# Kernel optimization log

Hardware: AMD Instinct MI355X
Metric: run time of the kernel (lower is better)

## Reference

```python
import jax, jax.numpy as jnp
import numpy as np

D_MODEL = 1024
N_HEADS = 16


def setup_inputs() -> dict:
    key = jax.random.key(0)
    ks = jax.random.split(key, 7)
    scale = 1.0 / np.sqrt(D_MODEL)
    seq = jax.random.normal(ks[0], (4, 1024, D_MODEL), dtype=jnp.float32)
    Wq = jax.random.normal(ks[1], (D_MODEL, D_MODEL), dtype=jnp.float32) * scale
    bq = jax.random.normal(ks[2], (D_MODEL,), dtype=jnp.float32) * 0.02
    Wk = jax.random.normal(ks[3], (D_MODEL, D_MODEL), dtype=jnp.float32) * scale
    bk = jax.random.normal(ks[4], (D_MODEL,), dtype=jnp.float32) * 0.02
    Wv = jax.random.normal(ks[5], (D_MODEL, D_MODEL), dtype=jnp.float32) * scale
    bv = jax.random.normal(ks[6], (D_MODEL,), dtype=jnp.float32) * 0.02
    return {"seq": seq, "Wq": Wq, "bq": bq, "Wk": Wk, "bk": bk, "Wv": Wv, "bv": bv}


def reference(seq, Wq, bq, Wk, bk, Wv, bv):
    B, S, D = seq.shape
    H = N_HEADS
    dv = D // H
    # nn.Linear: x @ W.T + b; W stored [out, in]
    q = (seq @ Wq.T + bq).reshape(B, S, H, dv).transpose(0, 2, 1, 3)  # [B,H,S,dv]
    k = (seq @ Wk.T + bk).reshape(B, S, H, dv).transpose(0, 2, 1, 3)
    v = (seq @ Wv.T + bv).reshape(B, S, H, dv).transpose(0, 2, 1, 3)
    scores = jnp.einsum('bhqd,bhkd->bhqk', q, k) / jnp.sqrt(jnp.asarray(dv, seq.dtype))
    p = jax.nn.softmax(scores, axis=-1)
    out = jnp.einsum('bhqk,bhkd->bhqd', p, v)  # [B,H,S,dv]
    return out.transpose(0, 2, 1, 3).reshape(B, S, D)
```

## Files before the change

### kernel.cpp

```cpp
#include <hip/hip_runtime.h>
#include <hip/hip_fp16.h>

typedef _Float16 f16x8 __attribute__((ext_vector_type(8)));
typedef _Float16 f16x4 __attribute__((ext_vector_type(4)));
typedef float f32x4 __attribute__((ext_vector_type(4)));

#define D_MODEL 1024
#define SEQ 1024
#define BATCH 4
#define NH 16
#define DV 64
#define M_TOTAL (BATCH * SEQ)
#define QBLK 128

__device__ __forceinline__ void gload16(const _Float16* g, _Float16* lds) {
    __builtin_amdgcn_global_load_lds((const __attribute__((address_space(1))) void*)g,
                                     (__attribute__((address_space(3))) void*)lds,
                                     16, 0, 0);
}

__global__ void cvt_f32_f16(const float* __restrict__ s, _Float16* __restrict__ d, int n) {
    int i = (blockIdx.x * blockDim.x + threadIdx.x) * 8;
    if (i >= n) return;
    float4 a = *(const float4*)(s + i);
    float4 b = *(const float4*)(s + i + 4);
    f16x8 h;
    h[0] = (_Float16)a.x; h[1] = (_Float16)a.y; h[2] = (_Float16)a.z; h[3] = (_Float16)a.w;
    h[4] = (_Float16)b.x; h[5] = (_Float16)b.y; h[6] = (_Float16)b.z; h[7] = (_Float16)b.w;
    *(f16x8*)(d + i) = h;
}

__global__ void cvt3_f32_f16(const float* __restrict__ s0, const float* __restrict__ s1,
                             const float* __restrict__ s2, _Float16* __restrict__ d0,
                             _Float16* __restrict__ d1, _Float16* __restrict__ d2, int n) {
    const float* s = (blockIdx.y == 0) ? s0 : (blockIdx.y == 1 ? s1 : s2);
    _Float16*    d = (blockIdx.y == 0) ? d0 : (blockIdx.y == 1 ? d1 : d2);
    int i = (blockIdx.x * blockDim.x + threadIdx.x) * 8;
    if (i >= n) return;
    float4 a = *(const float4*)(s + i);
    float4 b = *(const float4*)(s + i + 4);
    f16x8 h;
    h[0] = (_Float16)a.x; h[1] = (_Float16)a.y; h[2] = (_Float16)a.z; h[3] = (_Float16)a.w;
    h[4] = (_Float16)b.x; h[5] = (_Float16)b.y; h[6] = (_Float16)b.z; h[7] = (_Float16)b.w;
    *(f16x8*)(d + i) = h;
}

__global__ __launch_bounds__(512, 2) void qkv_gemm(
    const _Float16* __restrict__ X,
    const _Float16* __restrict__ W0, const _Float16* __restrict__ W1, const _Float16* __restrict__ W2,
    const float* __restrict__ b0, const float* __restrict__ b1, const float* __restrict__ b2,
    _Float16* __restrict__ Qo, _Float16* __restrict__ Ko, _Float16* __restrict__ Vto)
{
    __shared__ _Float16 SM[4 * 256 * 64];
#define ABASE(buf) (SM + (buf) * 16384)
#define BBASE(buf) (SM + 32768 + (buf) * 16384)

    const int tid = threadIdx.x;
    const int l = tid & 63;
    const int w = tid >> 6;
    const int wr = w >> 2, wc = w & 3;

    const int bid = blockIdx.x;
    const int nid = (bid & 7) * 24 + (bid >> 3);
    const int mt = nid & 15, ntg = nid >> 4;
    const int mat = ntg >> 2, nt = ntg & 3;
    const _Float16* Wm  = (mat == 0) ? W0 : (mat == 1 ? W1 : W2);
    const float*    bia = (mat == 0) ? b0 : (mat == 1 ? b1 : b2);
    const int m0 = mt * 256, n0 = nt * 256;

    const int str = tid >> 3;
    const int sc8 = ((tid & 7) ^ (str & 7)) * 8;
    const _Float16* xsrc = X  + (size_t)(m0 + str) * D_MODEL + sc8;
    const _Float16* wsrc = Wm + (size_t)(n0 + str) * D_MODEL + sc8;
    const int ldst = str * 64 + (tid & 7) * 8;

#define SA(buf, kt, h) do { \
    gload16(xsrc + (size_t)((h) * 128) * D_MODEL + (kt) * 64, ABASE(buf) + (h) * 8192 + ldst); \
    gload16(xsrc + (size_t)((h) * 128 + 64) * D_MODEL + (kt) * 64, ABASE(buf) + (h) * 8192 + 4096 + ldst); } while (0)
#define SB(buf, kt, h) do { \
    gload16(wsrc + (size_t)((h) * 128) * D_MODEL + (kt) * 64, BBASE(buf) + (h) * 8192 + ldst); \
    gload16(wsrc + (size_t)((h) * 128 + 64) * D_MODEL + (kt) * 64, BBASE(buf) + (h) * 8192 + 4096 + ldst); } while (0)

    const int fr = l & 15, g = l >> 4, fr7 = l & 7;
    const int wrow = wr * 128, bcol = wc * 64;

    f32x4 acc[8][4] = {};
    f16x8 b[4][2];

    SB(0, 0, 0); SB(0, 0, 1);
    SA(0, 0, 0); SA(0, 0, 1);
    SB(1, 1, 0); SB(1, 1, 1);
    asm volatile("s_waitcnt vmcnt(4)" ::: "memory");
    __builtin_amdgcn_s_barrier();

#define PHASES(BUF, TSA_BUF, TSA, TSB_BUF, TSB)                                              \
    _Pragma("unroll")                                                                        \
    for (int p = 0; p < 4; ++p) {                                                            \
        if (p == 0) {                                                                        \
            _Pragma("unroll")                                                                \
            for (int nj = 0; nj < 4; ++nj) {                                                 \
                const int rb = (bcol + nj * 16 + fr) * 64;                                   \
                b[nj][0] = *(const f16x8*)&BBASE(BUF)[rb + ((g ^ fr7) << 3)];                \
                b[nj][1] = *(const f16x8*)&BBASE(BUF)[rb + (((4 + g) ^ fr7) << 3)];          \
            }                                                                                \
        }                                                                                    \
        f16x8 aq[2][2];                                                                      \
        _Pragma("unroll")                                                                    \
        for (int q = 0; q < 2; ++q) {                                                        \
            const int ra = (wrow + (2 * p + q) * 16 + fr) * 64;                              \
            aq[q][0] = *(const f16x8*)&ABASE(BUF)[ra + ((g ^ fr7) << 3)];                    \
            aq[q][1] = *(const f16x8*)&ABASE(BUF)[ra + (((4 + g) ^ fr7) << 3)];              \
        }                                                                                    \
        if (p == 0) SA(TSA_BUF, TSA, 0);                                                     \
        else if (p == 1) SA(TSA_BUF, TSA, 1);                                                \
        else if (p == 2) SB(TSB_BUF, TSB, 0);                                                \
        else SB(TSB_BUF, TSB, 1);                                                            \
        __builtin_amdgcn_s_barrier();                                                        \
        __builtin_amdgcn_s_setprio(1);                                                       \
        _Pragma("unroll")                                                                    \
        for (int ks = 0; ks < 2; ++ks)                                                       \
            _Pragma("unroll")                                                                \
            for (int q = 0; q < 2; ++q)                                                      \
                _Pragma("unroll")                                                            \
                for (int nj = 0; nj < 4; ++nj)                                               \
                    acc[2 * p + q][nj] = __builtin_amdgcn_mfma_f32_16x16x32_f16(             \
                        aq[q][ks], b[nj][ks], acc[2 * p + q][nj], 0, 0, 0);                  \
        __builtin_amdgcn_s_setprio(0);                                                       \
        if (p == 3) asm volatile("s_waitcnt vmcnt(4)" ::: "memory");                         \
        __builtin_amdgcn_s_barrier();                                                        \
    }

    for (int it = 0; it < 8; ++it) {
        const int tA = 2 * it + 1;
        const int tN = (2 * it + 2 < 16) ? 2 * it + 2 : 15;
        const int tM = (2 * it + 3 < 16) ? 2 * it + 3 : 15;
        PHASES(0, 1, tA, 0, tN)
        PHASES(1, 0, tN, 1, tM)
    }
#undef PHASES
#undef SA
#undef SB

    if (mat != 2) {
        const float scale = (mat == 0) ? 0.125f * 1.44269504088896340736f : 1.0f;
#pragma unroll
        for (int nj = 0; nj < 4; ++nj) {
            const int o = n0 + bcol + nj * 16 + fr;
            const float bb = bia[o];
            const int h = o >> 6, dd = o & 63;
#pragma unroll
            for (int mi = 0; mi < 8; ++mi) {
#pragma unroll
                for (int r = 0; r < 4; ++r) {
                    const int m = m0 + wrow + mi * 16 + g * 4 + r;
                    const int bi = m >> 10, s = m & 1023;
                    const float v = (acc[mi][nj][r] + bb) * scale;
                    const _Float16 hv = (_Float16)v;
                    const int bh = bi * NH + h;
                    if (mat == 0) Qo[((size_t)bh * SEQ + s) * DV + dd] = hv;
                    else          Ko[((size_t)bh * SEQ + s) * DV + dd] = hv;
                }
            }
        }
    } else {
        asm volatile("s_waitcnt vmcnt(0)" ::: "memory");
        __syncthreads();
#pragma unroll
        for (int nj = 0; nj < 4; ++nj) {
            const int n = bcol + nj * 16 + fr;
            const float bb = bia[n0 + n];
#pragma unroll
            for (int mi = 0; mi < 8; ++mi) {
#pragma unroll
                for (int r = 0; r < 4; ++r) {
                    const int m = wrow + mi * 16 + g * 4 + r;
                    SM[n * 256 + ((((m >> 3) + n) & 31) << 3) + (m & 7)] =
                        (_Float16)(acc[mi][nj][r] + bb);
                }
            }
        }
        __syncthreads();
        const int bi = m0 >> 10, s0 = m0 & 1023;
#pragma unroll
        for (int itp = 0; itp < 16; ++itp) {
            const int task = itp * 512 + tid;
            const int dd = task >> 5, sc = task & 31;
            f16x8 vv = *(const f16x8*)&SM[dd * 256 + (((sc + dd) & 31) << 3)];
            const int og = n0 + dd;
            const int h = og >> 6, d = og & 63;
            const int bh = bi * NH + h;
            *(f16x8*)(Vto + ((size_t)bh * DV + d) * SEQ + s0 + sc * 8) = vv;
        }
    }
#undef ABASE
#undef BBASE
}

__global__ __launch_bounds__(256) void attn(
    const _Float16* __restrict__ Q, const _Float16* __restrict__ K,
    const _Float16* __restrict__ Vt, float* __restrict__ out)
{
    __shared__ _Float16 Kb[2][64 * 64];
    __shared__ _Float16 Vb[2][64 * 64];
    __shared__ _Float16 P[4][2][16][80];

    const int w = threadIdx.x >> 6, l = threadIdx.x & 63;
    const int qc = l & 15, g = l >> 4;

    const int fid = blockIdx.y * 8 + blockIdx.x;
    const int nid = (fid & 7) * 64 + (fid >> 3);
    const int bh = nid >> 3, qt = nid & 7;
    const int b = bh >> 4, h = bh & 15;
    const int q0 = qt * QBLK + w * 32;

    const int r8 = l >> 3;
    const int cs = ((l & 7) ^ r8) * 8;
    const _Float16* Kg = K  + (size_t)bh * SEQ * DV;
    const _Float16* Vg = Vt + (size_t)bh * DV * SEQ;

    f16x8 qf[2][2];
#pragma unroll
    for (int qg = 0; qg < 2; ++qg) {
        const _Float16* qp = Q + ((size_t)bh * SEQ + q0 + qg * 16 + qc) * DV + g * 8;
        qf[qg][0] = *(const f16x8*)(qp);
        qf[qg][1] = *(const f16x8*)(qp + 32);
    }

    float m_run[2] = {-1e30f, -1e30f}, l_run[2] = {0.f, 0.f};
    f32x4 oacc[2][4] = {};

#define STAGE(buf, kb)                                                          \
    {                                                                           \
        _Float16* kd = &Kb[buf][(w * 8) * 64];                                  \
        _Float16* vd = &Vb[buf][(w * 8) * 64];                                  \
        const int row = w * 8 + r8;                                             \
        gload16(Kg + (size_t)((kb) + row) * DV + cs, kd);                       \
        gload16(Kg + (size_t)((kb) + row + 32) * DV + cs, kd + 32 * 64);        \
        gload16(Vg + (size_t)row * SEQ + (kb) + cs, vd);                        \
        gload16(Vg + (size_t)(row + 32) * SEQ + (kb) + cs, vd + 32 * 64);       \
    }

    STAGE(0, 0);
    __syncthreads();

    for (int kt = 0; kt < 16; ++kt) {
        const int ct = kt & 1;
        if (kt < 15) STAGE(ct ^ 1, (kt + 1) * 64);
        const _Float16* Ktile = Kb[ct];
        const _Float16* Vtile = Vb[ct];

#pragma unroll
        for (int qg = 0; qg < 2; ++qg) {
            f32x4 sT[4];
            const f32x4 zf = {0.f, 0.f, 0.f, 0.f};
            __builtin_amdgcn_s_setprio(1);
#pragma unroll
            for (int kf = 0; kf < 4; ++kf) {
                const int row = kf * 16 + qc;
                f16x8 ka0 = *(const f16x8*)&Ktile[row * 64 + (((g)     ^ (qc & 7)) << 3)];
                f16x8 ka1 = *(const f16x8*)&Ktile[row * 64 + (((4 + g) ^ (qc & 7)) << 3)];
                f32x4 t = __builtin_amdgcn_mfma_f32_16x16x32_f16(ka0, qf[qg][0], zf, 0, 0, 0);
                sT[kf] = __builtin_amdgcn_mfma_f32_16x16x32_f16(ka1, qf[qg][1], t, 0, 0, 0);
            }
            __builtin_amdgcn_s_setprio(0);
            f32x4 mx = sT[0];
#pragma unroll
            for (int kf = 1; kf < 4; ++kf)
#pragma unroll
                for (int r = 0; r < 4; ++r) mx[r] = fmaxf(mx[r], sT[kf][r]);
            float pmax = fmaxf(fmaxf(mx[0], mx[1]), fmaxf(mx[2], mx[3]));
            pmax = fmaxf(pmax, __shfl_xor(pmax, 16));
            pmax = fmaxf(pmax, __shfl_xor(pmax, 32));
            if (!__all(pmax - m_run[qg] <= 8.0f)) {
                const float mn = fmaxf(m_run[qg], pmax);
                const float al = exp2f(m_run[qg] - mn);
                l_run[qg] *= al;
#pragma unroll
                for (int df = 0; df < 4; ++df) oacc[qg][df] *= al;
                m_run[qg] = mn;
            }
            float rsum = 0.f;
#pragma unroll
            for (int kf = 0; kf < 4; ++kf) {
                f16x4 ph;
#pragma unroll
                for (int r = 0; r < 4; ++r) {
                    const float p = exp2f(sT[kf][r] - m_run[qg]);
                    rsum += p;
                    ph[r] = (_Float16)p;
                }
                *(f16x4*)&P[w][qg][qc][kf * 16 + g * 4] = ph;
            }
            rsum += __shfl_xor(rsum, 16);
            rsum += __shfl_xor(rsum, 32);
            l_run[qg] += rsum;

            __builtin_amdgcn_s_setprio(1);
#pragma unroll
            for (int ks = 0; ks < 2; ++ks) {
                f16x8 pb = *(const f16x8*)&P[w][qg][qc][ks * 32 + g * 8];
#pragma unroll
                for (int df = 0; df < 4; ++df) {
                    const int row = df * 16 + qc;
                    f16x8 va = *(const f16x8*)&Vtile[row * 64 + (((ks * 4 + g) ^ (qc & 7)) << 3)];
                    oacc[qg][df] = __builtin_amdgcn_mfma_f32_16x16x32_f16(va, pb, oacc[qg][df], 0, 0, 0);
                }
            }
            __builtin_amdgcn_s_setprio(0);
        }
        __syncthreads();
    }
#undef STAGE

#pragma unroll
    for (int qg = 0; qg < 2; ++qg) {
        const float inv = 1.0f / l_run[qg];
        float* ob = out + ((size_t)b * SEQ + q0 + qg * 16 + qc) * D_MODEL + h * DV;
#pragma unroll
        for (int df = 0; df < 4; ++df) {
            float4 v4;
            v4.x = oacc[qg][df][0] * inv; v4.y = oacc[qg][df][1] * inv;
            v4.z = oacc[qg][df][2] * inv; v4.w = oacc[qg][df][3] * inv;
            *(float4*)(ob + df * 16 + g * 4) = v4;
        }
    }
}

extern "C" void kernel_launch(void* const* d_in, const int* in_sizes, int n_in,
                              void* d_out, int out_size, void* d_ws, size_t ws_size,
                              hipStream_t stream) {
    const float* seq = (const float*)d_in[0];
    const float* Wq  = (const float*)d_in[1];
    const float* bq  = (const float*)d_in[2];
    const float* Wk  = (const float*)d_in[3];
    const float* bk  = (const float*)d_in[4];
    const float* Wv  = (const float*)d_in[5];
    const float* bv  = (const float*)d_in[6];
    float* out = (float*)d_out;

    _Float16* seqh = (_Float16*)d_ws;
    _Float16* wqh  = seqh + (size_t)M_TOTAL * D_MODEL;
    _Float16* wkh  = wqh + (size_t)D_MODEL * D_MODEL;
    _Float16* wvh  = wkh + (size_t)D_MODEL * D_MODEL;
    _Float16* Qh   = wvh + (size_t)D_MODEL * D_MODEL;
    _Float16* Kh   = Qh + (size_t)M_TOTAL * D_MODEL;
    _Float16* Vth  = Kh + (size_t)M_TOTAL * D_MODEL;

    const int n_seq = M_TOTAL * D_MODEL;
    const int n_w   = D_MODEL * D_MODEL;
    cvt_f32_f16<<<n_seq / (256 * 8), 256, 0, stream>>>(seq, seqh, n_seq);
    cvt3_f32_f16<<<dim3(n_w / (256 * 8), 3), 256, 0, stream>>>(Wq, Wk, Wv, wqh, wkh, wvh, n_w);

    qkv_gemm<<<192, 512, 0, stream>>>(
        seqh, wqh, wkh, wvh, bq, bk, bv, Qh, Kh, Vth);

    attn<<<dim3(SEQ / QBLK, BATCH * NH), 256, 0, stream>>>(Qh, Kh, Vth, out);
}
```

Baseline: 91.81 us.

## Split attention KV range across two wave groups and pass P via lane shuffles

The attention kernel doubles to 512 threads. Two groups of four waves each process half of the key/value sequence for the same query block, and their partial softmax states are merged at the end through shared memory (split-K flash attention). The P matrix is converted with packed cvt_pkrtz and redistributed into MFMA operand layout through cross-lane shuffles instead of an LDS round trip. Both query groups' QK and PV MFMAs are interleaved for more independent instructions. The intent is to raise occupancy and latency hiding. The cost is more LDS, a final merge step, and extra shuffle work.

```diff
diff --git a/kernel.cpp b/kernel.cpp
--- a/kernel.cpp
+++ b/kernel.cpp
@@ -17,6 +17,13 @@
     __builtin_amdgcn_global_load_lds((const __attribute__((address_space(1))) void*)g,
                                      (__attribute__((address_space(3))) void*)lds,
                                      16, 0, 0);
+}
+
+__device__ __forceinline__ unsigned pk16(float a, float b) {
+    auto h = __builtin_amdgcn_cvt_pkrtz(a, b);
+    unsigned r;
+    __builtin_memcpy(&r, &h, 4);
+    return r;
 }
 
 __global__ void cvt_f32_f16(const float* __restrict__ s, _Float16* __restrict__ d, int n) {
@@ -196,27 +203,33 @@
 #undef BBASE
 }
 
-__global__ __launch_bounds__(256) void attn(
+__global__ __launch_bounds__(512, 4) void attn(
     const _Float16* __restrict__ Q, const _Float16* __restrict__ K,
     const _Float16* __restrict__ Vt, float* __restrict__ out)
 {
-    __shared__ _Float16 Kb[2][64 * 64];
-    __shared__ _Float16 Vb[2][64 * 64];
-    __shared__ _Float16 P[4][2][16][80];
-
-    const int w = threadIdx.x >> 6, l = threadIdx.x & 63;
+    __shared__ _Float16 Kb[2][2][64 * 64];
+    __shared__ _Float16 Vb[2][2][64 * 64];
+    __shared__ float MLb[4][2][16][2];
+
+    const int tid = threadIdx.x;
+    const int w = tid >> 6, l = tid & 63;
+    const int grp = w >> 2, wl = w & 3;
     const int qc = l & 15, g = l >> 4;
+    const int g0 = g & 1, g1 = g >> 1;
 
     const int fid = blockIdx.y * 8 + blockIdx.x;
     const int nid = (fid & 7) * 64 + (fid >> 3);
     const int bh = nid >> 3, qt = nid & 7;
     const int b = bh >> 4, h = bh & 15;
-    const int q0 = qt * QBLK + w * 32;
-
-    const int r8 = l >> 3;
-    const int cs = ((l & 7) ^ r8) * 8;
+    const int q0 = qt * QBLK + wl * 32;
+
+    const int gt = tid & 255;
+    const int srow = gt >> 3;
+    const int scs = ((gt & 7) ^ (srow & 7)) * 8;
+    const int ldst = srow * 64 + (gt & 7) * 8;
     const _Float16* Kg = K  + (size_t)bh * SEQ * DV;
     const _Float16* Vg = Vt + (size_t)bh * DV * SEQ;
+    const int kbase = grp * 512;
 
     f16x8 qf[2][2];
 #pragma unroll
@@ -229,45 +242,47 @@
     float m_run[2] = {-1e30f, -1e30f}, l_run[2] = {0.f, 0.f};
     f32x4 oacc[2][4] = {};
 
-#define STAGE(buf, kb)                                                          \
-    {                                                                           \
-        _Float16* kd = &Kb[buf][(w * 8) * 64];                                  \
-        _Float16* vd = &Vb[buf][(w * 8) * 64];                                  \
-        const int row = w * 8 + r8;                                             \
-        gload16(Kg + (size_t)((kb) + row) * DV + cs, kd);                       \
-        gload16(Kg + (size_t)((kb) + row + 32) * DV + cs, kd + 32 * 64);        \
-        gload16(Vg + (size_t)row * SEQ + (kb) + cs, vd);                        \
-        gload16(Vg + (size_t)(row + 32) * SEQ + (kb) + cs, vd + 32 * 64);       \
-    }
+#define STAGE(buf, kt) do {                                                        \
+        const int kb = kbase + (kt) * 64;                                          \
+        gload16(Kg + (size_t)(kb + srow) * DV + scs, &Kb[grp][buf][0] + ldst);     \
+        gload16(Kg + (size_t)(kb + srow + 32) * DV + scs, &Kb[grp][buf][2048] + ldst); \
+        gload16(Vg + (size_t)srow * SEQ + kb + scs, &Vb[grp][buf][0] + ldst);      \
+        gload16(Vg + (size_t)(srow + 32) * SEQ + kb + scs, &Vb[grp][buf][2048] + ldst); \
+    } while (0)
 
     STAGE(0, 0);
     __syncthreads();
 
-    for (int kt = 0; kt < 16; ++kt) {
+    for (int kt = 0; kt < 8; ++kt) {
         const int ct = kt & 1;
-        if (kt < 15) STAGE(ct ^ 1, (kt + 1) * 64);
-        const _Float16* Ktile = Kb[ct];
-        const _Float16* Vtile = Vb[ct];
-
+        if (kt < 7) STAGE(ct ^ 1, kt + 1);
+        const _Float16* Ktile = &Kb[grp][ct][0];
+        const _Float16* Vtile = &Vb[grp][ct][0];
+
+        f32x4 sT[2][4];
+        const f32x4 zf = {0.f, 0.f, 0.f, 0.f};
+        __builtin_amdgcn_s_setprio(1);
+#pragma unroll
+        for (int kf = 0; kf < 4; ++kf) {
+            const int row = kf * 16 + qc;
+            f16x8 ka0 = *(const f16x8*)&Ktile[row * 64 + (((g)     ^ (qc & 7)) << 3)];
+            f16x8 ka1 = *(const f16x8*)&Ktile[row * 64 + (((4 + g) ^ (qc & 7)) << 3)];
+#pragma unroll
+            for (int qg = 0; qg < 2; ++qg) {
+                f32x4 t = __builtin_amdgcn_mfma_f32_16x16x32_f16(ka0, qf[qg][0], zf, 0, 0, 0);
+                sT[qg][kf] = __builtin_amdgcn_mfma_f32_16x16x32_f16(ka1, qf[qg][1], t, 0, 0, 0);
+            }
+        }
+        __builtin_amdgcn_s_setprio(0);
+
+        f16x8 pb[2][2];
 #pragma unroll
         for (int qg = 0; qg < 2; ++qg) {
-            f32x4 sT[4];
-            const f32x4 zf = {0.f, 0.f, 0.f, 0.f};
-            __builtin_amdgcn_s_setprio(1);
-#pragma unroll
-            for (int kf = 0; kf < 4; ++kf) {
-                const int row = kf * 16 + qc;
-                f16x8 ka0 = *(const f16x8*)&Ktile[row * 64 + (((g)     ^ (qc & 7)) << 3)];
-                f16x8 ka1 = *(const f16x8*)&Ktile[row * 64 + (((4 + g) ^ (qc & 7)) << 3)];
-                f32x4 t = __builtin_amdgcn_mfma_f32_16x16x32_f16(ka0, qf[qg][0], zf, 0, 0, 0);
-                sT[kf] = __builtin_amdgcn_mfma_f32_16x16x32_f16(ka1, qf[qg][1], t, 0, 0, 0);
-            }
-            __builtin_amdgcn_s_setprio(0);
-            f32x4 mx = sT[0];
+            f32x4 mx = sT[qg][0];
 #pragma unroll
             for (int kf = 1; kf < 4; ++kf)
 #pragma unroll
-                for (int r = 0; r < 4; ++r) mx[r] = fmaxf(mx[r], sT[kf][r]);
+                for (int r = 0; r < 4; ++r) mx[r] = fmaxf(mx[r], sT[qg][kf][r]);
             float pmax = fmaxf(fmaxf(mx[0], mx[1]), fmaxf(mx[2], mx[3]));
             pmax = fmaxf(pmax, __shfl_xor(pmax, 16));
             pmax = fmaxf(pmax, __shfl_xor(pmax, 32));
@@ -280,48 +295,93 @@
                 m_run[qg] = mn;
             }
             float rsum = 0.f;
+            unsigned u[4][2];
 #pragma unroll
             for (int kf = 0; kf < 4; ++kf) {
-                f16x4 ph;
-#pragma unroll
-                for (int r = 0; r < 4; ++r) {
-                    const float p = exp2f(sT[kf][r] - m_run[qg]);
-                    rsum += p;
-                    ph[r] = (_Float16)p;
-                }
-                *(f16x4*)&P[w][qg][qc][kf * 16 + g * 4] = ph;
+                const float p0 = exp2f(sT[qg][kf][0] - m_run[qg]);
+                const float p1 = exp2f(sT[qg][kf][1] - m_run[qg]);
+                const float p2 = exp2f(sT[qg][kf][2] - m_run[qg]);
+                const float p3 = exp2f(sT[qg][kf][3] - m_run[qg]);
+                rsum += (p0 + p1) + (p2 + p3);
+                u[kf][0] = pk16(p0, p1);
+                u[kf][1] = pk16(p2, p3);
             }
             rsum += __shfl_xor(rsum, 16);
             rsum += __shfl_xor(rsum, 32);
             l_run[qg] += rsum;
 
-            __builtin_amdgcn_s_setprio(1);
+            unsigned keep[2][2], rec[2][2];
+#pragma unroll
+            for (int ks = 0; ks < 2; ++ks)
+#pragma unroll
+                for (int rp = 0; rp < 2; ++rp) {
+                    const unsigned own0  = g1 ? u[2 * ks + 1][rp] : u[2 * ks][rp];
+                    const unsigned send1 = g1 ? u[2 * ks][rp]     : u[2 * ks + 1][rp];
+                    const unsigned recv0 = (unsigned)__shfl_xor((int)send1, 32);
+                    const unsigned km = (g1 == g0) ? own0 : recv0;
+                    const unsigned sp = (g1 == g0) ? recv0 : own0;
+                    rec[ks][rp] = (unsigned)__shfl_xor((int)sp, 16);
+                    keep[ks][rp] = km;
+                }
 #pragma unroll
             for (int ks = 0; ks < 2; ++ks) {
-                f16x8 pb = *(const f16x8*)&P[w][qg][qc][ks * 32 + g * 8];
-#pragma unroll
-                for (int df = 0; df < 4; ++df) {
-                    const int row = df * 16 + qc;
-                    f16x8 va = *(const f16x8*)&Vtile[row * 64 + (((ks * 4 + g) ^ (qc & 7)) << 3)];
-                    oacc[qg][df] = __builtin_amdgcn_mfma_f32_16x16x32_f16(va, pb, oacc[qg][df], 0, 0, 0);
-                }
-            }
-            __builtin_amdgcn_s_setprio(0);
-        }
+                unsigned wd[4];
+                wd[0] = g0 ? rec[ks][0]  : keep[ks][0];
+                wd[1] = g0 ? rec[ks][1]  : keep[ks][1];
+                wd[2] = g0 ? keep[ks][0] : rec[ks][0];
+                wd[3] = g0 ? keep[ks][1] : rec[ks][1];
+                __builtin_memcpy(&pb[qg][ks], wd, 16);
+            }
+        }
+
+        __builtin_amdgcn_s_setprio(1);
+#pragma unroll
+        for (int ks = 0; ks < 2; ++ks)
+#pragma unroll
+            for (int df = 0; df < 4; ++df) {
+                const int row = df * 16 + qc;
+                f16x8 va = *(const f16x8*)&Vtile[row * 64 + (((ks * 4 + g) ^ (qc & 7)) << 3)];
+                oacc[0][df] = __builtin_amdgcn_mfma_f32_16x16x32_f16(va, pb[0][ks], oacc[0][df], 0, 0, 0);
+                oacc[1][df] = __builtin_amdgcn_mfma_f32_16x16x32_f16(va, pb[1][ks], oacc[1][df], 0, 0, 0);
+            }
+        __builtin_amdgcn_s_setprio(0);
+
         __syncthreads();
     }
 #undef STAGE
 
-#pragma unroll
-    for (int qg = 0; qg < 2; ++qg) {
-        const float inv = 1.0f / l_run[qg];
-        float* ob = out + ((size_t)b * SEQ + q0 + qg * 16 + qc) * D_MODEL + h * DV;
-#pragma unroll
-        for (int df = 0; df < 4; ++df) {
-            float4 v4;
-            v4.x = oacc[qg][df][0] * inv; v4.y = oacc[qg][df][1] * inv;
-            v4.z = oacc[qg][df][2] * inv; v4.w = oacc[qg][df][3] * inv;
-            *(float4*)(ob + df * 16 + g * 4) = v4;
+    float* Ob = (float*)&Vb[0][0][0];
+    if (grp == 1) {
+#pragma unroll
+        for (int qg = 0; qg < 2; ++qg) {
+            float* ob = Ob + (wl * 2 + qg) * 1024 + qc * 64;
+#pragma unroll
+            for (int df = 0; df < 4; ++df)
+                *(f32x4*)(ob + df * 16 + g * 4) = oacc[qg][df];
+            if (g == 0) {
+                MLb[wl][qg][qc][0] = m_run[qg];
+                MLb[wl][qg][qc][1] = l_run[qg];
+            }
+        }
+    }
+    __syncthreads();
+    if (grp == 0) {
+#pragma unroll
+        for (int qg = 0; qg < 2; ++qg) {
+            const float m1 = MLb[wl][qg][qc][0];
+            const float l1 = MLb[wl][qg][qc][1];
+            const float M  = fmaxf(m_run[qg], m1);
+            const float e0 = exp2f(m_run[qg] - M);
+            const float e1 = exp2f(m1 - M);
+            const float inv = 1.0f / (e0 * l_run[qg] + e1 * l1);
+            const float* ob = Ob + (wl * 2 + qg) * 1024 + qc * 64;
+            float* op = out + ((size_t)b * SEQ + q0 + qg * 16 + qc) * D_MODEL + h * DV;
+#pragma unroll
+            for (int df = 0; df < 4; ++df) {
+                f32x4 o1 = *(const f32x4*)(ob + df * 16 + g * 4);
+                f32x4 r = (oacc[qg][df] * e0 + o1 * e1) * inv;
+                *(f32x4*)(op + df * 16 + g * 4) = r;
+            }
         }
     }
 }
@@ -354,5 +414,5 @@
     qkv_gemm<<<192, 512, 0, stream>>>(
         seqh, wqh, wkh, wvh, bq, bk, bv, Qh, Kh, Vth);
 
-    attn<<<dim3(SEQ / QBLK, BATCH * NH), 256, 0, stream>>>(Qh, Kh, Vth, out);
-}
+    attn<<<dim3(SEQ / QBLK, BATCH * NH), 512, 0, stream>>>(Qh, Kh, Vth, out);
+}
```

Result: faster. 87.00 us (-5.2%).

## Drop LDS staging in attention; load K/V straight to registers, shuffle P

Applied to the files above, without the earlier changes.

The attention kernel no longer stages K and V tiles through double-buffered shared memory. Each wave loads its K and V fragments directly from global memory into registers, prefetching the next K tile while computing the current one. The probability matrix is repacked between the QK and PV MFMA layouts with cross-lane shuffles instead of a round trip through LDS, which also removes the block-wide barriers. In exchange, every wave now fetches the whole K/V tile itself with no sharing across waves, raising global/L2 traffic and register pressure; a launch bound of 2 is added to cap registers.

```diff
diff --git a/kernel.cpp b/kernel.cpp
--- a/kernel.cpp
+++ b/kernel.cpp
@@ -17,6 +17,13 @@
     __builtin_amdgcn_global_load_lds((const __attribute__((address_space(1))) void*)g,
                                      (__attribute__((address_space(3))) void*)lds,
                                      16, 0, 0);
+}
+
+__device__ __forceinline__ unsigned pk16(float a, float b) {
+    auto h = __builtin_amdgcn_cvt_pkrtz(a, b);
+    unsigned r;
+    __builtin_memcpy(&r, &h, 4);
+    return r;
 }
 
 __global__ void cvt_f32_f16(const float* __restrict__ s, _Float16* __restrict__ d, int n) {
@@ -196,16 +203,14 @@
 #undef BBASE
 }
 
-__global__ __launch_bounds__(256) void attn(
+__global__ __launch_bounds__(256, 2) void attn(
     const _Float16* __restrict__ Q, const _Float16* __restrict__ K,
     const _Float16* __restrict__ Vt, float* __restrict__ out)
 {
-    __shared__ _Float16 Kb[2][64 * 64];
-    __shared__ _Float16 Vb[2][64 * 64];
-    __shared__ _Float16 P[4][2][16][80];
-
-    const int w = threadIdx.x >> 6, l = threadIdx.x & 63;
+    const int tid = threadIdx.x;
+    const int w = tid >> 6, l = tid & 63;
     const int qc = l & 15, g = l >> 4;
+    const int g0 = g & 1, g1 = g >> 1;
 
     const int fid = blockIdx.y * 8 + blockIdx.x;
     const int nid = (fid & 7) * 64 + (fid >> 3);
@@ -213,8 +218,6 @@
     const int b = bh >> 4, h = bh & 15;
     const int q0 = qt * QBLK + w * 32;
 
-    const int r8 = l >> 3;
-    const int cs = ((l & 7) ^ r8) * 8;
     const _Float16* Kg = K  + (size_t)bh * SEQ * DV;
     const _Float16* Vg = Vt + (size_t)bh * DV * SEQ;
 
@@ -229,99 +232,135 @@
     float m_run[2] = {-1e30f, -1e30f}, l_run[2] = {0.f, 0.f};
     f32x4 oacc[2][4] = {};
 
-#define STAGE(buf, kb)                                                          \
-    {                                                                           \
-        _Float16* kd = &Kb[buf][(w * 8) * 64];                                  \
-        _Float16* vd = &Vb[buf][(w * 8) * 64];                                  \
-        const int row = w * 8 + r8;                                             \
-        gload16(Kg + (size_t)((kb) + row) * DV + cs, kd);                       \
-        gload16(Kg + (size_t)((kb) + row + 32) * DV + cs, kd + 32 * 64);        \
-        gload16(Vg + (size_t)row * SEQ + (kb) + cs, vd);                        \
-        gload16(Vg + (size_t)(row + 32) * SEQ + (kb) + cs, vd + 32 * 64);       \
-    }
-
-    STAGE(0, 0);
-    __syncthreads();
-
-    for (int kt = 0; kt < 16; ++kt) {
-        const int ct = kt & 1;
-        if (kt < 15) STAGE(ct ^ 1, (kt + 1) * 64);
-        const _Float16* Ktile = Kb[ct];
-        const _Float16* Vtile = Vb[ct];
-
-#pragma unroll
-        for (int qg = 0; qg < 2; ++qg) {
-            f32x4 sT[4];
-            const f32x4 zf = {0.f, 0.f, 0.f, 0.f};
-            __builtin_amdgcn_s_setprio(1);
-#pragma unroll
-            for (int kf = 0; kf < 4; ++kf) {
-                const int row = kf * 16 + qc;
-                f16x8 ka0 = *(const f16x8*)&Ktile[row * 64 + (((g)     ^ (qc & 7)) << 3)];
-                f16x8 ka1 = *(const f16x8*)&Ktile[row * 64 + (((4 + g) ^ (qc & 7)) << 3)];
-                f32x4 t = __builtin_amdgcn_mfma_f32_16x16x32_f16(ka0, qf[qg][0], zf, 0, 0, 0);
-                sT[kf] = __builtin_amdgcn_mfma_f32_16x16x32_f16(ka1, qf[qg][1], t, 0, 0, 0);
-            }
-            __builtin_amdgcn_s_setprio(0);
-            f32x4 mx = sT[0];
-#pragma unroll
-            for (int kf = 1; kf < 4; ++kf)
-#pragma unroll
-                for (int r = 0; r < 4; ++r) mx[r] = fmaxf(mx[r], sT[kf][r]);
-            float pmax = fmaxf(fmaxf(mx[0], mx[1]), fmaxf(mx[2], mx[3]));
-            pmax = fmaxf(pmax, __shfl_xor(pmax, 16));
-            pmax = fmaxf(pmax, __shfl_xor(pmax, 32));
-            if (!__all(pmax - m_run[qg] <= 8.0f)) {
-                const float mn = fmaxf(m_run[qg], pmax);
-                const float al = exp2f(m_run[qg] - mn);
-                l_run[qg] *= al;
-#pragma unroll
-                for (int df = 0; df < 4; ++df) oacc[qg][df] *= al;
-                m_run[qg] = mn;
-            }
-            float rsum = 0.f;
-#pragma unroll
-            for (int kf = 0; kf < 4; ++kf) {
-                f16x4 ph;
-#pragma unroll
-                for (int r = 0; r < 4; ++r) {
-                    const float p = exp2f(sT[kf][r] - m_run[qg]);
-                    rsum += p;
-                    ph[r] = (_Float16)p;
-                }
-                *(f16x4*)&P[w][qg][qc][kf * 16 + g * 4] = ph;
-            }
-            rsum += __shfl_xor(rsum, 16);
-            rsum += __shfl_xor(rsum, 32);
-            l_run[qg] += rsum;
-
-            __builtin_amdgcn_s_setprio(1);
-#pragma unroll
-            for (int ks = 0; ks < 2; ++ks) {
-                f16x8 pb = *(const f16x8*)&P[w][qg][qc][ks * 32 + g * 8];
-#pragma unroll
-                for (int df = 0; df < 4; ++df) {
-                    const int row = df * 16 + qc;
-                    f16x8 va = *(const f16x8*)&Vtile[row * 64 + (((ks * 4 + g) ^ (qc & 7)) << 3)];
-                    oacc[qg][df] = __builtin_amdgcn_mfma_f32_16x16x32_f16(va, pb, oacc[qg][df], 0, 0, 0);
-                }
-            }
-            __builtin_amdgcn_s_setprio(0);
-        }
-        __syncthreads();
-    }
-#undef STAGE
+    f16x8 kA[8], kB[8];
+#pragma unroll
+    for (int kf = 0; kf < 4; ++kf) {
+        const _Float16* kp = Kg + (size_t)(kf * 16 + qc) * DV + g * 8;
+        kA[kf * 2]     = *(const f16x8*)(kp);
+        kA[kf * 2 + 1] = *(const f16x8*)(kp + 32);
+    }
+
+#define ABODY(KC, KN, t)                                                                     \
+    {                                                                                        \
+        const int kb = (t) * 64;                                                             \
+                                    \
+        f16x8 vr[2][4];                                                                      \
+        _Pragma("unroll")                                                                    \
+        for (int ks = 0; ks < 2; ++ks)                                                       \
+            _Pragma("unroll")                                                                \
+            for (int df = 0; df < 4; ++df)                                                   \
+                vr[ks][df] = *(const f16x8*)(Vg + (size_t)(df * 16 + qc) * SEQ + kb +        \
+                                             ks * 32 + g * 8);                               \
+                                        \
+        f32x4 sT[2][4];                                                                      \
+        const f32x4 zf = {0.f, 0.f, 0.f, 0.f};                                               \
+        __builtin_amdgcn_s_setprio(1);                                                       \
+        _Pragma("unroll")                                                                    \
+        for (int kf = 0; kf < 4; ++kf)                                                       \
+            _Pragma("unroll")                                                                \
+            for (int qg = 0; qg < 2; ++qg) {                                                 \
+                f32x4 tt = __builtin_amdgcn_mfma_f32_16x16x32_f16(KC[2 * kf], qf[qg][0],     \
+                                                                  zf, 0, 0, 0);             \
+                sT[qg][kf] = __builtin_amdgcn_mfma_f32_16x16x32_f16(KC[2 * kf + 1],          \
+                                                                    qf[qg][1], tt, 0, 0, 0); \
+            }                                                                                \
+        __builtin_amdgcn_s_setprio(0);                                                       \
+                       \
+        const int tn = ((t) + 1 < 16) ? (t) + 1 : 15;                                        \
+        _Pragma("unroll")                                                                    \
+        for (int kf = 0; kf < 4; ++kf) {                                                     \
+            const _Float16* kp = Kg + (size_t)(tn * 64 + kf * 16 + qc) * DV + g * 8;         \
+            KN[kf * 2]     = *(const f16x8*)(kp);                                            \
+            KN[kf * 2 + 1] = *(const f16x8*)(kp + 32);                                       \
+        }                                                                                    \
+                                                       \
+        f16x8 pb[2][2];                                                                      \
+        _Pragma("unroll")                                                                    \
+        for (int qg = 0; qg < 2; ++qg) {                                                     \
+            f32x4 mx = sT[qg][0];                                                            \
+            _Pragma("unroll")                                                                \
+            for (int kf = 1; kf < 4; ++kf)                                                   \
+                _Pragma("unroll")                                                            \
+                for (int r = 0; r < 4; ++r) mx[r] = fmaxf(mx[r], sT[qg][kf][r]);             \
+            float pmax = fmaxf(fmaxf(mx[0], mx[1]), fmaxf(mx[2], mx[3]));                    \
+            pmax = fmaxf(pmax, __shfl_xor(pmax, 16));                                        \
+            pmax = fmaxf(pmax, __shfl_xor(pmax, 32));                                        \
+            if (!__all(pmax - m_run[qg] <= 8.0f)) {                                          \
+                const float mn = fmaxf(m_run[qg], pmax);                                     \
+                const float al = exp2f(m_run[qg] - mn);                                      \
+                l_run[qg] *= al;                                                             \
+                _Pragma("unroll")                                                            \
+                for (int df = 0; df < 4; ++df) oacc[qg][df] *= al;                           \
+                m_run[qg] = mn;                                                              \
+            }                                                                                \
+            float rsum = 0.f;                                                                \
+            unsigned u[4][2];                                                                \
+            _Pragma("unroll")                                                                \
+            for (int kf = 0; kf < 4; ++kf) {                                                 \
+                const float p0 = exp2f(sT[qg][kf][0] - m_run[qg]);                           \
+                const float p1 = exp2f(sT[qg][kf][1] - m_run[qg]);                           \
+                const float p2 = exp2f(sT[qg][kf][2] - m_run[qg]);                           \
+                const float p3 = exp2f(sT[qg][kf][3] - m_run[qg]);                           \
+                rsum += (p0 + p1) + (p2 + p3);                                               \
+                u[kf][0] = pk16(p0, p1);                                                     \
+                u[kf][1] = pk16(p2, p3);                                                     \
+            }                                                                                \
+            rsum += __shfl_xor(rsum, 16);                                                    \
+            rsum += __shfl_xor(rsum, 32);                                                    \
+            l_run[qg] += rsum;                                                               \
+            unsigned keep[2][2], rec[2][2];                                                  \
+            _Pragma("unroll")                                                                \
+            for (int ks = 0; ks < 2; ++ks)                                                   \
+                _Pragma("unroll")                                                            \
+                for (int rp = 0; rp < 2; ++rp) {                                             \
+                    const unsigned own0  = g1 ? u[2 * ks + 1][rp] : u[2 * ks][rp];           \
+                    const unsigned send1 = g1 ? u[2 * ks][rp]     : u[2 * ks + 1][rp];       \
+                    const unsigned recv0 = (unsigned)__shfl_xor((int)send1, 32);             \
+                    const unsigned km = (g1 == g0) ? own0 : recv0;                           \
+                    const unsigned sp = (g1 == g0) ? recv0 : own0;                           \
+                    rec[ks][rp] = (unsigned)__shfl_xor((int)sp, 16);                         \
+                    keep[ks][rp] = km;                                                       \
+                }                                                                            \
+            _Pragma("unroll")                                                                \
+            for (int ks = 0; ks < 2; ++ks) {                                                 \
+                unsigned wd[4];                                                              \
+                wd[0] = g0 ? rec[ks][0]  : keep[ks][0];                                      \
+                wd[1] = g0 ? rec[ks][1]  : keep[ks][1];                                      \
+                wd[2] = g0 ? keep[ks][0] : rec[ks][0];                                       \
+                wd[3] = g0 ? keep[ks][1] : rec[ks][1];                                       \
+                __builtin_memcpy(&pb[qg][ks], wd, 16);                                       \
+            }                                                                                \
+        }                                                                                    \
+                                                           \
+        __builtin_amdgcn_s_setprio(1);                                                       \
+        _Pragma("unroll")                                                                    \
+        for (int ks = 0; ks < 2; ++ks)                                                       \
+            _Pragma("unroll")                                                                \
+            for (int df = 0; df < 4; ++df) {                                                 \
+                oacc[0][df] = __builtin_amdgcn_mfma_f32_16x16x32_f16(vr[ks][df], pb[0][ks],  \
+                                                                     oacc[0][df], 0, 0, 0);  \
+                oacc[1][df] = __builtin_amdgcn_mfma_f32_16x16x32_f16(vr[ks][df], pb[1][ks],  \
+                                                                     oacc[1][df], 0, 0, 0);  \
+            }                                                                                \
+        __builtin_amdgcn_s_setprio(0);                                                       \
+    }
+
+    for (int kt2 = 0; kt2 < 8; ++kt2) {
+        ABODY(kA, kB, 2 * kt2)
+        ABODY(kB, kA, 2 * kt2 + 1)
+    }
+#undef ABODY
 
 #pragma unroll
     for (int qg = 0; qg < 2; ++qg) {
         const float inv = 1.0f / l_run[qg];
-        float* ob = out + ((size_t)b * SEQ + q0 + qg * 16 + qc) * D_MODEL + h * DV;
+        float* op = out + ((size_t)b * SEQ + q0 + qg * 16 + qc) * D_MODEL + h * DV;
 #pragma unroll
         for (int df = 0; df < 4; ++df) {
+            f32x4 r = oacc[qg][df] * inv;
             float4 v4;
-            v4.x = oacc[qg][df][0] * inv; v4.y = oacc[qg][df][1] * inv;
-            v4.z = oacc[qg][df][2] * inv; v4.w = oacc[qg][df][3] * inv;
-            *(float4*)(ob + df * 16 + g * 4) = v4;
+            v4.x = r[0]; v4.y = r[1]; v4.z = r[2]; v4.w = r[3];
+            *(float4*)(op + df * 16 + g * 4) = v4;
         }
     }
 }
```

Result: slower. 109.9 us (+19.7%).
